# Performance work log

Measured on AMD Instinct MI355X. Metric: run time of the kernel, lower is better.

Reference implementation:

```python
import jax, jax.numpy as jnp
import numpy as np

N, E, G = 100000, 1600000, 256
F_IN, HID, NCLS = 16, 64, 2
EPS = 1e-5


def segment_mean(v, seg, num_segments):
    s = jax.ops.segment_sum(v, seg, num_segments=num_segments)
    c = jax.ops.segment_sum(jnp.ones((v.shape[0], 1), v.dtype), seg, num_segments=num_segments)
    return s / jnp.maximum(c, 1.0)


def graph_norm(x, seg, weight, bias, mean_scale):
    # PyG GraphNorm: per-graph mean/var with learnable mean_scale
    mean = segment_mean(x, seg, G)                      # [G, C]
    centered = x - mean_scale * mean[seg]               # [N, C]
    var = segment_mean(centered * centered, seg, G)     # [G, C]
    return weight * centered * jax.lax.rsqrt(var[seg] + EPS) + bias


def gcn_conv(x, W, b, row, col, n):
    # PyG GCNConv: h = x @ W; symmetric norm with added self-loops; scatter-add; + bias
    h = x @ W                                           # [N, C_out]
    deg = jnp.zeros((n,), x.dtype).at[row].add(1.0) + 1.0  # +1 self-loop
    dinv = jax.lax.rsqrt(deg)
    norm = (dinv[row] * dinv[col])[:, None]             # [E, 1]
    agg = jnp.zeros_like(h).at[row].add(norm * h[col])  # neighbor messages
    agg = agg + (dinv * dinv)[:, None] * h              # self-loop messages
    return agg + b


def setup_inputs():
    key = jax.random.key(0)
    ks = jax.random.split(key, 16)
    x = jax.random.normal(ks[0], (N, F_IN), jnp.float32)
    edge_index = jax.random.randint(ks[1], (2, E), 0, N, jnp.int32)
    batch = jnp.sort(jax.random.randint(ks[2], (N,), 0, G, jnp.int32))
    s = lambda k, shp: jax.random.normal(k, shp, jnp.float32) * 0.05
    return {
        "x": x, "edge_index": edge_index, "batch": batch,
        "gn0_w": jnp.ones((F_IN,)), "gn0_b": jnp.zeros((F_IN,)), "gn0_ms": jnp.ones((F_IN,)),
        "W1": s(ks[3], (F_IN, HID)), "b1": jnp.zeros((HID,)),
        "gn1_w": jnp.ones((HID,)), "gn1_b": jnp.zeros((HID,)), "gn1_ms": jnp.ones((HID,)),
        "W2": s(ks[4], (HID, HID)), "b2": jnp.zeros((HID,)),
        "gn2_w": jnp.ones((HID,)), "gn2_b": jnp.zeros((HID,)), "gn2_ms": jnp.ones((HID,)),
        "W3": s(ks[5], (HID, HID)), "b3": jnp.zeros((HID,)),
        "Wd": s(ks[6], (HID, HID)), "bd": jnp.zeros((HID,)),
        "Wo": s(ks[7], (HID, NCLS)), "bo": jnp.zeros((NCLS,)),
    }


def reference(x, edge_index, batch, gn0_w, gn0_b, gn0_ms, W1, b1, gn1_w, gn1_b, gn1_ms,
              W2, b2, gn2_w, gn2_b, gn2_ms, W3, b3, Wd, bd, Wo, bo):
    row, col = edge_index[0], edge_index[1]
    h = graph_norm(x, batch, gn0_w, gn0_b, gn0_ms)
    h = jax.nn.relu(gcn_conv(h, W1, b1, row, col, N))
    h = graph_norm(h, batch, gn1_w, gn1_b, gn1_ms)
    h = jax.nn.relu(gcn_conv(h, W2, b2, row, col, N))
    h = graph_norm(h, batch, gn2_w, gn2_b, gn2_ms)
    h = jax.nn.relu(gcn_conv(h, W3, b3, row, col, N))
    g = segment_mean(h, batch, G)                       # global_mean_pool -> [G, HID]
    # dropout is identity in eval mode
    g = jax.nn.relu(g @ Wd + bd)
    logits = g @ Wo + bo
    return jax.nn.softmax(logits, axis=1)
```

## Files before the change

kernel.cpp:

```cpp
#include <hip/hip_runtime.h>
#include <hip/hip_bf16.h>

#define NN 100000
#define NE 1600000
#define NG 256
#define FIN 16
#define HID 64
#define NBK 391
#define NTILE 391
#define PMAX 4864
#define MAXT (NN / 16 + NG)

__device__ __forceinline__ int lower_bound_i(const int* __restrict__ b, int n, int v) {
    int lo = 0, hi = n;
    while (lo < hi) { int m = (lo + hi) >> 1; if (b[m] < v) lo = m + 1; else hi = m; }
    return lo;
}

__device__ __forceinline__ unsigned pack_bf16(float a, float b) {
    unsigned ua = __float_as_uint(a), ub = __float_as_uint(b);
    ua = (ua + 0x7fffu + ((ua >> 16) & 1u)) >> 16;
    ub = (ub + 0x7fffu + ((ub >> 16) & 1u)) & 0xffff0000u;
    return ua | ub;
}
#define BF_LO(u) __uint_as_float((u) << 16)
#define BF_HI(u) __uint_as_float((u) & 0xffff0000u)

typedef __attribute__((ext_vector_type(8))) short bf16x8;
typedef __attribute__((ext_vector_type(4))) float f32x4;
union FU { uint4 u; bf16x8 v; };

__global__ __launch_bounds__(512) void k_zb(int* __restrict__ bhist) {
    bhist[threadIdx.x] = 0;
}

__global__ __launch_bounds__(512) void k_bhist(const int4* __restrict__ row4, int* __restrict__ bhist) {
    __shared__ int h[NBK];
    for (int i = threadIdx.x; i < NBK; i += 512) h[i] = 0;
    __syncthreads();
    int t0 = blockIdx.x * 1024 + threadIdx.x;
#pragma unroll
    for (int it = 0; it < 2; ++it) {
        int t = t0 + it * 512;
        if (t < NE / 4) {
            int4 r = row4[t];
            atomicAdd(&h[r.x >> 8], 1); atomicAdd(&h[r.y >> 8], 1);
            atomicAdd(&h[r.z >> 8], 1); atomicAdd(&h[r.w >> 8], 1);
        }
    }
    __syncthreads();
    for (int i = threadIdx.x; i < NBK; i += 512)
        if (h[i]) atomicAdd(&bhist[i], h[i]);
}

__global__ __launch_bounds__(512) void k_bscan(const int* __restrict__ bhist, int* __restrict__ bbase,
                                               int* __restrict__ bcur) {
    __shared__ int sc[512];
    int t = threadIdx.x;
    int v = (t < NBK) ? bhist[t] : 0;
    sc[t] = v;
    __syncthreads();
    int acc = v;
    for (int off = 1; off < 512; off <<= 1) {
        int add = (t >= off) ? sc[t - off] : 0;
        __syncthreads();
        acc += add;
        sc[t] = acc;
        __syncthreads();
    }
    if (t < NBK) { bbase[t] = acc - v; bcur[t] = acc - v; }
    if (t == NBK - 1) bbase[NBK] = acc;
}

__global__ __launch_bounds__(512) void k_bscatter(const int4* __restrict__ row4, const int4* __restrict__ col4,
                                                  int* __restrict__ bcur, int2* __restrict__ pairs) {
    __shared__ int lh[NBK], lofs[NBK], lbase[NBK], lc[NBK];
    __shared__ int sc[512];
    __shared__ int2 stg[4096];
    for (int i = threadIdx.x; i < NBK; i += 512) { lh[i] = 0; lc[i] = 0; }
    __syncthreads();
    int t0 = blockIdx.x * 1024 + threadIdx.x;
#pragma unroll
    for (int it = 0; it < 2; ++it) {
        int t = t0 + it * 512;
        if (t < NE / 4) {
            int4 r = row4[t];
            atomicAdd(&lh[r.x >> 8], 1); atomicAdd(&lh[r.y >> 8], 1);
            atomicAdd(&lh[r.z >> 8], 1); atomicAdd(&lh[r.w >> 8], 1);
        }
    }
    __syncthreads();
    {
        int t = threadIdx.x;
        int v = (t < NBK) ? lh[t] : 0;
        sc[t] = v;
        __syncthreads();
        int acc = v;
        for (int off = 1; off < 512; off <<= 1) {
            int add = (t >= off) ? sc[t - off] : 0;
            __syncthreads();
            acc += add;
            sc[t] = acc;
            __syncthreads();
        }
        if (t < NBK) lofs[t] = acc - v;
    }
    if (threadIdx.x < NBK) {
        int c = lh[threadIdx.x];
        lbase[threadIdx.x] = c ? atomicAdd(&bcur[threadIdx.x], c) : 0;
    }
    __syncthreads();
#pragma unroll
    for (int it = 0; it < 2; ++it) {
        int t = t0 + it * 512;
        if (t < NE / 4) {
            int4 r = row4[t];
            int4 c = col4[t];
            int b, rk;
            b = r.x >> 8; rk = atomicAdd(&lc[b], 1); stg[lofs[b] + rk] = make_int2(r.x, c.x);
            b = r.y >> 8; rk = atomicAdd(&lc[b], 1); stg[lofs[b] + rk] = make_int2(r.y, c.y);
            b = r.z >> 8; rk = atomicAdd(&lc[b], 1); stg[lofs[b] + rk] = make_int2(r.z, c.z);
            b = r.w >> 8; rk = atomicAdd(&lc[b], 1); stg[lofs[b] + rk] = make_int2(r.w, c.w);
        }
    }
    __syncthreads();
    int nv = min(4096, NE - blockIdx.x * 4096);
    for (int j = threadIdx.x; j < nv; j += 512) {
        int2 p = stg[j];
        int b = p.x >> 8;
        pairs[lbase[b] + (j - lofs[b])] = p;
    }
}

__global__ __launch_bounds__(256) void k_bsort(const int2* __restrict__ pairs, const int* __restrict__ bbase,
                                               int* __restrict__ csr_col, int* __restrict__ startv,
                                               int* __restrict__ degc, float* __restrict__ dinv) {
    __shared__ int2 prs[PMAX];
    __shared__ int colo[PMAX];
    __shared__ int cnt[256], ofs[256], c2[256], sc[256];
    int b = blockIdx.x;
    int s = bbase[b];
    int n = min(bbase[b + 1] - s, PMAX);
    cnt[threadIdx.x] = 0;
    c2[threadIdx.x] = 0;
    __syncthreads();
    for (int i = threadIdx.x; i < n; i += 256) {
        int2 p = pairs[s + i];
        prs[i] = p;
        atomicAdd(&cnt[p.x & 255], 1);
    }
    __syncthreads();
    {
        int t = threadIdx.x, v = cnt[t];
        sc[t] = v;
        __syncthreads();
        int acc = v;
        for (int off = 1; off < 256; off <<= 1) {
            int add = (t >= off) ? sc[t - off] : 0;
            __syncthreads();
            acc += add;
            sc[t] = acc;
            __syncthreads();
        }
        ofs[t] = acc - v;
    }
    __syncthreads();
    for (int i = threadIdx.x; i < n; i += 256) {
        int2 p = prs[i];
        int lr = p.x & 255;
        int rk = atomicAdd(&c2[lr], 1);
        colo[ofs[lr] + rk] = p.y;
    }
    __syncthreads();
    for (int i = threadIdx.x; i < n; i += 256) csr_col[s + i] = colo[i];
    int r = (b << 8) + threadIdx.x;
    if (r < NN) {
        int c = cnt[threadIdx.x];
        startv[r] = s + ofs[threadIdx.x];
        degc[r] = c;
        dinv[r] = rsqrtf((float)(c + 1));
    }
}

__global__ __launch_bounds__(256) void k_setup(const int* __restrict__ batch, int* __restrict__ ntot,
                                               int* __restrict__ tg, int* __restrict__ tbase,
                                               int* __restrict__ tcnt, const float* __restrict__ W1,
                                               unsigned* __restrict__ Wt1p) {
    if (blockIdx.x == 1) {
        int t = threadIdx.x;
        int j = t >> 2, kq = t & 3;
#pragma unroll
        for (int i = 0; i < 4; i++) {
            int idx = kq * 4 + i;
            int k = idx * 2;
            unsigned v = 0;
            if (k < FIN) v = pack_bf16(W1[k * 64 + j], W1[(k + 1) * 64 + j]);
            Wt1p[j * 16 + idx] = v;
        }
        return;
    }
    __shared__ int gst[NG + 1];
    __shared__ int sc[NG];
    int t = threadIdx.x;
    gst[t] = lower_bound_i(batch, NN, t);
    if (t == 0) gst[NG] = NN;
    __syncthreads();
    int ng = gst[t + 1] - gst[t];
    int nt = (ng + 15) >> 4;
    sc[t] = nt;
    __syncthreads();
    int acc = nt;
    for (int off = 1; off < NG; off <<= 1) {
        int add = (t >= off) ? sc[t - off] : 0;
        __syncthreads();
        acc += add;
        sc[t] = acc;
        __syncthreads();
    }
    int ofs = acc - nt;
    for (int i = 0; i < nt; i++) {
        tg[ofs + i] = t;
        tbase[ofs + i] = gst[t] + i * 16;
        tcnt[ofs + i] = min(16, ng - i * 16);
    }
    if (t == NG - 1) ntot[0] = acc;
}

__global__ __launch_bounds__(256) void k_graphnorm16(const float* __restrict__ x, const int* __restrict__ batch,
                              const float* __restrict__ w, const float* __restrict__ b,
                              const float* __restrict__ ms, const float* __restrict__ dinv,
                              unsigned* __restrict__ xb) {
    constexpr int C = FIN, NPB = 256 / C;
    __shared__ float red[NPB][C], red2[NPB][C];
    __shared__ float mm_s[C], rs_s[C];
    int g = blockIdx.x;
    int s = lower_bound_i(batch, NN, g);
    int e = lower_bound_i(batch, NN, g + 1);
    float fc = (float)max(e - s, 1);
    int c = threadIdx.x % C, slot = threadIdx.x / C;

    float a1 = 0.f, a2 = 0.f;
    for (int i = s + slot; i < e; i += NPB) { float v = x[i * C + c]; a1 += v; a2 += v * v; }
    red[slot][c] = a1;
    red2[slot][c] = a2;
    __syncthreads();
    if (threadIdx.x < C) {
        float t1 = 0.f, t2 = 0.f;
        for (int k = 0; k < NPB; k++) { t1 += red[k][threadIdx.x]; t2 += red2[k][threadIdx.x]; }
        float mean = t1 / fc;
        float mm = ms[threadIdx.x] * mean;
        float var = t2 / fc - 2.f * mm * mean + mm * mm;
        mm_s[threadIdx.x] = mm;
        rs_s[threadIdx.x] = rsqrtf(var + 1e-5f);
    }
    __syncthreads();
    float mm = mm_s[c], ww = w[c] * rs_s[c], bb = b[c];
    for (int i = s + slot; i < e; i += NPB) {
        float v = (ww * (x[i * C + c] - mm) + bb) * dinv[i];
        float partner = __shfl_xor(v, 1);
        if ((c & 1) == 0) xb[(long)i * 8 + (c >> 1)] = pack_bf16(v, partner);
    }
}

__global__ __launch_bounds__(256) void k_gnstats2(const unsigned* __restrict__ xw, const int* __restrict__ batch,
                          const float* __restrict__ w, const float* __restrict__ b,
                          const float* __restrict__ ms, const float* __restrict__ W,
                          unsigned* __restrict__ Wtp, float* __restrict__ bias2) {
    constexpr int C = 64, NPB = 4;
    __shared__ float red[NPB][C], red2[NPB][C];
    __shared__ float sA[C], sB[C];
    int g = blockIdx.x;
    int s = lower_bound_i(batch, NN, g);
    int e = lower_bound_i(batch, NN, g + 1);
    float fc = (float)max(e - s, 1);
    int c = threadIdx.x & 63, slot = threadIdx.x >> 6;

    float a1 = 0.f, a2 = 0.f;
    for (int i = s + slot; i < e; i += NPB) {
        unsigned u = xw[(long)i * 32 + (c >> 1)];
        float v = (c & 1) ? BF_HI(u) : BF_LO(u);
        a1 += v; a2 += v * v;
    }
    red[slot][c] = a1;
    red2[slot][c] = a2;
    __syncthreads();
    if (threadIdx.x < C) {
        float t1 = 0.f, t2 = 0.f;
        for (int k = 0; k < NPB; k++) { t1 += red[k][threadIdx.x]; t2 += red2[k][threadIdx.x]; }
        float mean = t1 / fc;
        float mm = ms[threadIdx.x] * mean;
        float var = t2 / fc - 2.f * mm * mean + mm * mm;
        float A = w[threadIdx.x] * rsqrtf(var + 1e-5f);
        sA[threadIdx.x] = A;
        sB[threadIdx.x] = b[threadIdx.x] - A * mm;
    }
    __syncthreads();
    int j = threadIdx.x >> 2, kq = threadIdx.x & 3;
    unsigned* wrow = Wtp + ((long)g * 64 + j) * 32 + kq * 8;
    float part = 0.f;
#pragma unroll
    for (int i = 0; i < 8; i++) {
        int k = kq * 16 + 2 * i;
        float w0 = W[k * 64 + j], w1 = W[(k + 1) * 64 + j];
        wrow[i] = pack_bf16(sA[k] * w0, sA[k + 1] * w1);
        part += sB[k] * w0 + sB[k + 1] * w1;
    }
    part += __shfl_xor(part, 1);
    part += __shfl_xor(part, 2);
    if (kq == 0) bias2[g * 64 + j] = part;
}

__global__ __launch_bounds__(256) void k_gather16(const unsigned* __restrict__ xb, const int* __restrict__ startv,
                           const int* __restrict__ degc, const float* __restrict__ dinv,
                           const int* __restrict__ csr_col, unsigned* __restrict__ agg) {
    int wave = (blockIdx.x * blockDim.x + threadIdx.x) >> 6;
    if (wave >= NN) return;
    int lane = threadIdx.x & 63;
    int p = lane & 7, g = lane >> 3;
    int s = startv[wave], cnt = degc[wave];
    float di = dinv[wave];
    float ax = 0.f, ay = 0.f;
    int k = g;
    for (; k + 8 < cnt; k += 16) {
        int c0 = csr_col[s + k], c1 = csr_col[s + k + 8];
        unsigned u0 = xb[(long)c0 * 8 + p], u1 = xb[(long)c1 * 8 + p];
        ax += BF_LO(u0) + BF_LO(u1);
        ay += BF_HI(u0) + BF_HI(u1);
    }
    for (; k < cnt; k += 8) {
        int c0 = csr_col[s + k];
        unsigned u0 = xb[(long)c0 * 8 + p];
        ax += BF_LO(u0);
        ay += BF_HI(u0);
    }
    ax += __shfl_xor(ax, 8);  ay += __shfl_xor(ay, 8);
    ax += __shfl_xor(ax, 16); ay += __shfl_xor(ay, 16);
    ax += __shfl_xor(ax, 32); ay += __shfl_xor(ay, 32);
    if (g == 0) {
        unsigned u = xb[(long)wave * 8 + p];
        ax = (ax + BF_LO(u)) * di;
        ay = (ay + BF_HI(u)) * di;
        agg[(long)wave * 16 + p] = pack_bf16(ax, ay);
    } else if (g == 1) {
        agg[(long)wave * 16 + 8 + p] = 0u;
    }
}

template <int KU, bool PERG, bool RELU, bool DINV>
__global__ __launch_bounds__(256) void k_gemmT(const unsigned* __restrict__ Ain, const unsigned* __restrict__ Wt,
                        const float* __restrict__ biasv, const float* __restrict__ dinv,
                        const int* __restrict__ ntot, const int* __restrict__ tg,
                        const int* __restrict__ tbase, const int* __restrict__ tcnt,
                        unsigned* __restrict__ Aout) {
    const int RW = KU * 16;
    int tix = blockIdx.x * 4 + (threadIdx.x >> 6);
    if (tix >= ntot[0]) return;
    int g = tg[tix], base = tbase[tix], n = tcnt[tix];
    int l = threadIdx.x & 63, r = l & 15, q = l >> 4;
    FU a[KU];
#pragma unroll
    for (int s = 0; s < KU; s++) {
        if (r < n) a[s].u = *(const uint4*)(Ain + (long)(base + r) * RW + s * 16 + q * 4);
        else a[s].u = make_uint4(0, 0, 0, 0);
    }
    const unsigned* wb = PERG ? (Wt + (long)g * 64 * RW) : Wt;
    f32x4 acc[4];
#pragma unroll
    for (int t = 0; t < 4; t++) {
        acc[t] = (f32x4){0.f, 0.f, 0.f, 0.f};
#pragma unroll
        for (int s = 0; s < KU; s++) {
            FU bfrag;
            bfrag.u = *(const uint4*)(wb + (long)(t * 16 + r) * RW + s * 16 + q * 4);
            acc[t] = __builtin_amdgcn_mfma_f32_16x16x32_bf16(a[s].v, bfrag.v, acc[t], 0, 0, 0);
        }
    }
    const float* bb = PERG ? (biasv + g * 64) : biasv;
    float dv[4];
#pragma unroll
    for (int e = 0; e < 4; e++) {
        int node = base + q * 4 + e;
        dv[e] = DINV ? ((node < NN) ? dinv[node] : 0.f) : 1.f;
    }
#pragma unroll
    for (int t = 0; t < 4; t++) {
        float bv = bb[t * 16 + r];
#pragma unroll
        for (int e = 0; e < 4; e++) {
            float v = acc[t][e] + bv;
            if (RELU) v = fmaxf(v, 0.f);
            if (DINV) v *= dv[e];
            float part = __shfl_xor(v, 1);
            if ((q * 4 + e) < n && (r & 1) == 0)
                Aout[(long)(base + q * 4 + e) * 32 + t * 8 + (r >> 1)] = pack_bf16(v, part);
        }
    }
}

__global__ __launch_bounds__(256) void k_gather64(const unsigned* __restrict__ h2, const int* __restrict__ startv,
                           const int* __restrict__ degc, const float* __restrict__ dinv,
                           const int* __restrict__ csr_col, const float* __restrict__ bias,
                           unsigned* __restrict__ outp) {
    int wave = (blockIdx.x * blockDim.x + threadIdx.x) >> 6;
    if (wave >= NN) return;
    int lane = threadIdx.x & 63;
    int p = lane & 31, g = lane >> 5;
    int s = startv[wave], cnt = degc[wave];
    float di = dinv[wave];
    float ax = 0.f, ay = 0.f;
    if (g == 0) {
        unsigned u = h2[(long)wave * 32 + p];
        ax = BF_LO(u);
        ay = BF_HI(u);
    }
    for (int k = g * 8; k < cnt; k += 16) {
        int cc[8];
#pragma unroll
        for (int i = 0; i < 8; i++) {
            int idx = k + i;
            cc[i] = (idx < cnt) ? csr_col[s + idx] : -1;
        }
        unsigned u[8];
#pragma unroll
        for (int i = 0; i < 8; i++)
            u[i] = (cc[i] >= 0) ? h2[(long)cc[i] * 32 + p] : 0u;
#pragma unroll
        for (int i = 0; i < 8; i++) { ax += BF_LO(u[i]); ay += BF_HI(u[i]); }
    }
    ax += __shfl_xor(ax, 32);
    ay += __shfl_xor(ay, 32);
    if (g == 0) {
        float vx = fmaxf(ax * di + bias[2 * p], 0.f);
        float vy = fmaxf(ay * di + bias[2 * p + 1], 0.f);
        outp[(long)wave * 32 + p] = pack_bf16(vx, vy);
    }
}

__global__ __launch_bounds__(1024) void k_poolhead(const unsigned* __restrict__ xw, const int* __restrict__ batch,
                       const float* __restrict__ Wd, const float* __restrict__ bd,
                       const float* __restrict__ Wo, const float* __restrict__ bo,
                       float* __restrict__ out) {
    __shared__ float red[16][64];
    __shared__ float wds[64 * 64];
    __shared__ float gs[64];
    int g = blockIdx.x;
    int s = lower_bound_i(batch, NN, g);
    int e = lower_bound_i(batch, NN, g + 1);
    int c = threadIdx.x & 63, slot = threadIdx.x >> 6;
    for (int i = threadIdx.x; i < 64 * 64; i += 1024) wds[i] = Wd[i];
    float acc = 0.f;
    for (int i = s + slot; i < e; i += 16) {
        unsigned u = xw[(long)i * 32 + (c >> 1)];
        acc += (c & 1) ? BF_HI(u) : BF_LO(u);
    }
    red[slot][c] = acc;
    __syncthreads();
    if (threadIdx.x < 64) {
        float t = 0.f;
        for (int k = 0; k < 16; k++) t += red[k][threadIdx.x];
        gs[threadIdx.x] = t / (float)max(e - s, 1);
    }
    __syncthreads();
    if (threadIdx.x < 64) {
        int j = threadIdx.x;
        float a2 = bd[j];
        for (int k = 0; k < 64; k++) a2 += gs[k] * wds[k * 64 + j];
        float hv = fmaxf(a2, 0.f);
        float p0 = hv * Wo[j * 2 + 0], p1 = hv * Wo[j * 2 + 1];
        for (int off = 32; off; off >>= 1) { p0 += __shfl_down(p0, off); p1 += __shfl_down(p1, off); }
        if (j == 0) {
            float l0 = p0 + bo[0], l1 = p1 + bo[1];
            float m = fmaxf(l0, l1);
            float e0 = expf(l0 - m), e1 = expf(l1 - m);
            float inv = 1.f / (e0 + e1);
            out[g * 2 + 0] = e0 * inv;
            out[g * 2 + 1] = e1 * inv;
        }
    }
}

extern "C" void kernel_launch(void* const* d_in, const int* in_sizes, int n_in,
                              void* d_out, int out_size, void* d_ws, size_t ws_size,
                              hipStream_t stream) {
    const float* x = (const float*)d_in[0];
    const int* ei = (const int*)d_in[1];
    const int* row = ei;
    const int* col = ei + NE;
    const int* batch = (const int*)d_in[2];
    const float* gn0w = (const float*)d_in[3];
    const float* gn0b = (const float*)d_in[4];
    const float* gn0ms = (const float*)d_in[5];
    const float* W1 = (const float*)d_in[6];
    const float* b1 = (const float*)d_in[7];
    const float* gn1w = (const float*)d_in[8];
    const float* gn1b = (const float*)d_in[9];
    const float* gn1ms = (const float*)d_in[10];
    const float* W2 = (const float*)d_in[11];
    const float* b2 = (const float*)d_in[12];
    const float* gn2w = (const float*)d_in[13];
    const float* gn2b = (const float*)d_in[14];
    const float* gn2ms = (const float*)d_in[15];
    const float* W3 = (const float*)d_in[16];
    const float* b3 = (const float*)d_in[17];
    const float* Wd = (const float*)d_in[18];
    const float* bd = (const float*)d_in[19];
    const float* Wo = (const float*)d_in[20];
    const float* bo = (const float*)d_in[21];
    float* outp = (float*)d_out;

    int* bhist = (int*)d_ws;
    int* bbase = bhist + 512;
    int* bcur = bbase + 512;
    int* startv = bcur + 512;
    int* degc = startv + NN;
    float* dinv = (float*)(degc + NN);
    int* csr_col = (int*)(dinv + NN);
    int* ntot = csr_col + NE;
    int* tg = ntot + 16;
    int* tbase = tg + 6608;
    int* tcnt = tbase + 6608;
    unsigned* Wt1p = (unsigned*)(tcnt + 6608);
    unsigned* Wtp = Wt1p + 1024;
    float* bias2 = (float*)(Wtp + (long)NG * 64 * 32);
    unsigned* xb = (unsigned*)(bias2 + NG * 64);
    unsigned* agg16 = xb + (long)NN * 8;
    unsigned* bufA = agg16 + (long)NN * 16;
    unsigned* bufB = bufA + (long)NN * 32;
    unsigned* h2 = bufB + (long)NN * 32;
    int2* pairs = (int2*)bufA;

    const int NBG = (MAXT + 3) / 4;

    k_zb<<<1, 512, 0, stream>>>(bhist);
    k_bhist<<<NTILE, 512, 0, stream>>>((const int4*)row, bhist);
    k_bscan<<<1, 512, 0, stream>>>(bhist, bbase, bcur);
    k_bscatter<<<NTILE, 512, 0, stream>>>((const int4*)row, (const int4*)col, bcur, pairs);
    k_bsort<<<NBK, 256, 0, stream>>>(pairs, bbase, csr_col, startv, degc, dinv);

    k_setup<<<2, 256, 0, stream>>>(batch, ntot, tg, tbase, tcnt, W1, Wt1p);

    k_graphnorm16<<<NG, 256, 0, stream>>>(x, batch, gn0w, gn0b, gn0ms, dinv, xb);
    k_gather16<<<(NN * 64 + 255) / 256, 256, 0, stream>>>(xb, startv, degc, dinv, csr_col, agg16);
    k_gemmT<1, false, true, false><<<NBG, 256, 0, stream>>>(agg16, Wt1p, b1, dinv, ntot, tg, tbase, tcnt, bufA);

    k_gnstats2<<<NG, 256, 0, stream>>>(bufA, batch, gn1w, gn1b, gn1ms, W2, Wtp, bias2);
    k_gemmT<2, true, false, true><<<NBG, 256, 0, stream>>>(bufA, Wtp, bias2, dinv, ntot, tg, tbase, tcnt, h2);
    k_gather64<<<(NN * 64 + 255) / 256, 256, 0, stream>>>(h2, startv, degc, dinv, csr_col, b2, bufB);

    k_gnstats2<<<NG, 256, 0, stream>>>(bufB, batch, gn2w, gn2b, gn2ms, W3, Wtp, bias2);
    k_gemmT<2, true, false, true><<<NBG, 256, 0, stream>>>(bufB, Wtp, bias2, dinv, ntot, tg, tbase, tcnt, h2);
    k_gather64<<<(NN * 64 + 255) / 256, 256, 0, stream>>>(h2, startv, degc, dinv, csr_col, b3, bufA);

    k_poolhead<<<NG, 1024, 0, stream>>>(bufA, batch, Wd, bd, Wo, bo, outp);
}
```

Measured before the change: 414.0 us.

## Pad CSR rows to multiples of four with sentinel zero rows for vectorized gathers

The CSR build in k_bsort now pads each row's neighbor list to a multiple of four, filling the padding with a sentinel index NN. A zero row is written at index NN of the feature buffers, so the gathers can load column indices as uint4 and skip bounds checks and the scalar tail loops. Alongside this, the graph-norm and stats kernels move to 512-thread blocks with packed float4 reductions, and the zeroing kernel is replaced by hipMemsetAsync. The padding adds storage and gather work for the padded slots, and k_bsort no longer stages pairs in LDS, so it reads them from global memory twice.

New measurement: 382.3 us. 1.08x faster.

```diff
diff --git a/kernel.cpp b/kernel.cpp
--- a/kernel.cpp
+++ b/kernel.cpp
@@ -9,6 +9,7 @@
 #define NBK 391
 #define NTILE 391
 #define PMAX 4864
+#define BMAXP 5632
 #define MAXT (NN / 16 + NG)
 
 __device__ __forceinline__ int lower_bound_i(const int* __restrict__ b, int n, int v) {
@@ -29,10 +30,6 @@
 typedef __attribute__((ext_vector_type(8))) short bf16x8;
 typedef __attribute__((ext_vector_type(4))) float f32x4;
 union FU { uint4 u; bf16x8 v; };
-
-__global__ __launch_bounds__(512) void k_zb(int* __restrict__ bhist) {
-    bhist[threadIdx.x] = 0;
-}
 
 __global__ __launch_bounds__(512) void k_bhist(const int4* __restrict__ row4, int* __restrict__ bhist) {
     __shared__ int h[NBK];
@@ -135,23 +132,21 @@
 __global__ __launch_bounds__(256) void k_bsort(const int2* __restrict__ pairs, const int* __restrict__ bbase,
                                                int* __restrict__ csr_col, int* __restrict__ startv,
                                                int* __restrict__ degc, float* __restrict__ dinv) {
-    __shared__ int2 prs[PMAX];
-    __shared__ int colo[PMAX];
-    __shared__ int cnt[256], ofs[256], c2[256], sc[256];
+    __shared__ int colo[BMAXP];
+    __shared__ int cnt[256], pofs[256], c2[256], sc[256];
     int b = blockIdx.x;
     int s = bbase[b];
     int n = min(bbase[b + 1] - s, PMAX);
     cnt[threadIdx.x] = 0;
     c2[threadIdx.x] = 0;
     __syncthreads();
-    for (int i = threadIdx.x; i < n; i += 256) {
-        int2 p = pairs[s + i];
-        prs[i] = p;
-        atomicAdd(&cnt[p.x & 255], 1);
-    }
-    __syncthreads();
+    for (int i = threadIdx.x; i < n; i += 256)
+        atomicAdd(&cnt[pairs[s + i].x & 255], 1);
+    __syncthreads();
+    int c = cnt[threadIdx.x];
+    int pc = (c + 3) & ~3;
     {
-        int t = threadIdx.x, v = cnt[t];
+        int t = threadIdx.x, v = pc;
         sc[t] = v;
         __syncthreads();
         int acc = v;
@@ -162,22 +157,25 @@
             sc[t] = acc;
             __syncthreads();
         }
-        ofs[t] = acc - v;
-    }
+        pofs[t] = acc - v;
+    }
+    __syncthreads();
+    int ptot = sc[255];
+    for (int i = threadIdx.x; i < ptot; i += 256) colo[i] = NN;
     __syncthreads();
     for (int i = threadIdx.x; i < n; i += 256) {
-        int2 p = prs[i];
+        int2 p = pairs[s + i];
         int lr = p.x & 255;
         int rk = atomicAdd(&c2[lr], 1);
-        colo[ofs[lr] + rk] = p.y;
-    }
-    __syncthreads();
-    for (int i = threadIdx.x; i < n; i += 256) csr_col[s + i] = colo[i];
+        colo[pofs[lr] + rk] = p.y;
+    }
+    __syncthreads();
+    int gb = b * BMAXP;
+    for (int i = threadIdx.x; i < ptot; i += 256) csr_col[gb + i] = colo[i];
     int r = (b << 8) + threadIdx.x;
     if (r < NN) {
-        int c = cnt[threadIdx.x];
-        startv[r] = s + ofs[threadIdx.x];
-        degc[r] = c;
+        startv[r] = gb + pofs[threadIdx.x];
+        degc[r] = pc;
         dinv[r] = rsqrtf((float)(c + 1));
     }
 }
@@ -185,7 +183,8 @@
 __global__ __launch_bounds__(256) void k_setup(const int* __restrict__ batch, int* __restrict__ ntot,
                                                int* __restrict__ tg, int* __restrict__ tbase,
                                                int* __restrict__ tcnt, const float* __restrict__ W1,
-                                               unsigned* __restrict__ Wt1p) {
+                                               unsigned* __restrict__ Wt1p, unsigned* __restrict__ xb,
+                                               unsigned* __restrict__ h2) {
     if (blockIdx.x == 1) {
         int t = threadIdx.x;
         int j = t >> 2, kq = t & 3;
@@ -197,6 +196,8 @@
             if (k < FIN) v = pack_bf16(W1[k * 64 + j], W1[(k + 1) * 64 + j]);
             Wt1p[j * 16 + idx] = v;
         }
+        if (t < 32) h2[(long)NN * 32 + t] = 0u;
+        if (t < 8) xb[(long)NN * 8 + t] = 0u;
         return;
     }
     __shared__ int gst[NG + 1];
@@ -226,11 +227,11 @@
     if (t == NG - 1) ntot[0] = acc;
 }
 
-__global__ __launch_bounds__(256) void k_graphnorm16(const float* __restrict__ x, const int* __restrict__ batch,
+__global__ __launch_bounds__(512) void k_graphnorm16(const float* __restrict__ x, const int* __restrict__ batch,
                               const float* __restrict__ w, const float* __restrict__ b,
                               const float* __restrict__ ms, const float* __restrict__ dinv,
                               unsigned* __restrict__ xb) {
-    constexpr int C = FIN, NPB = 256 / C;
+    constexpr int C = FIN, NPB = 512 / C;
     __shared__ float red[NPB][C], red2[NPB][C];
     __shared__ float mm_s[C], rs_s[C];
     int g = blockIdx.x;
@@ -262,52 +263,57 @@
     }
 }
 
-__global__ __launch_bounds__(256) void k_gnstats2(const unsigned* __restrict__ xw, const int* __restrict__ batch,
+__global__ __launch_bounds__(512) void k_gnstats2(const unsigned* __restrict__ xw, const int* __restrict__ batch,
                           const float* __restrict__ w, const float* __restrict__ b,
                           const float* __restrict__ ms, const float* __restrict__ W,
                           unsigned* __restrict__ Wtp, float* __restrict__ bias2) {
-    constexpr int C = 64, NPB = 4;
-    __shared__ float red[NPB][C], red2[NPB][C];
-    __shared__ float sA[C], sB[C];
+    __shared__ float4 red[16][32];
+    __shared__ float sA[64], sB[64];
     int g = blockIdx.x;
     int s = lower_bound_i(batch, NN, g);
     int e = lower_bound_i(batch, NN, g + 1);
     float fc = (float)max(e - s, 1);
-    int c = threadIdx.x & 63, slot = threadIdx.x >> 6;
-
-    float a1 = 0.f, a2 = 0.f;
-    for (int i = s + slot; i < e; i += NPB) {
-        unsigned u = xw[(long)i * 32 + (c >> 1)];
-        float v = (c & 1) ? BF_HI(u) : BF_LO(u);
-        a1 += v; a2 += v * v;
-    }
-    red[slot][c] = a1;
-    red2[slot][c] = a2;
-    __syncthreads();
-    if (threadIdx.x < C) {
+    int cu = threadIdx.x & 31, slot = threadIdx.x >> 5;
+
+    float s1l = 0.f, s1h = 0.f, s2l = 0.f, s2h = 0.f;
+    for (int i = s + slot; i < e; i += 16) {
+        unsigned u = xw[(long)i * 32 + cu];
+        float lo = BF_LO(u), hi = BF_HI(u);
+        s1l += lo; s1h += hi; s2l += lo * lo; s2h += hi * hi;
+    }
+    red[slot][cu] = make_float4(s1l, s1h, s2l, s2h);
+    __syncthreads();
+    if (threadIdx.x < 64) {
+        int cc = threadIdx.x, iu = cc >> 1, hi = cc & 1;
         float t1 = 0.f, t2 = 0.f;
-        for (int k = 0; k < NPB; k++) { t1 += red[k][threadIdx.x]; t2 += red2[k][threadIdx.x]; }
+        for (int k = 0; k < 16; k++) {
+            float4 v = red[k][iu];
+            t1 += hi ? v.y : v.x;
+            t2 += hi ? v.w : v.z;
+        }
         float mean = t1 / fc;
-        float mm = ms[threadIdx.x] * mean;
+        float mm = ms[cc] * mean;
         float var = t2 / fc - 2.f * mm * mean + mm * mm;
-        float A = w[threadIdx.x] * rsqrtf(var + 1e-5f);
-        sA[threadIdx.x] = A;
-        sB[threadIdx.x] = b[threadIdx.x] - A * mm;
-    }
-    __syncthreads();
-    int j = threadIdx.x >> 2, kq = threadIdx.x & 3;
-    unsigned* wrow = Wtp + ((long)g * 64 + j) * 32 + kq * 8;
-    float part = 0.f;
-#pragma unroll
-    for (int i = 0; i < 8; i++) {
-        int k = kq * 16 + 2 * i;
-        float w0 = W[k * 64 + j], w1 = W[(k + 1) * 64 + j];
-        wrow[i] = pack_bf16(sA[k] * w0, sA[k + 1] * w1);
-        part += sB[k] * w0 + sB[k + 1] * w1;
-    }
-    part += __shfl_xor(part, 1);
-    part += __shfl_xor(part, 2);
-    if (kq == 0) bias2[g * 64 + j] = part;
+        float A = w[cc] * rsqrtf(var + 1e-5f);
+        sA[cc] = A;
+        sB[cc] = b[cc] - A * mm;
+    }
+    __syncthreads();
+    if (threadIdx.x < 256) {
+        int j = threadIdx.x >> 2, kq = threadIdx.x & 3;
+        unsigned* wrow = Wtp + ((long)g * 64 + j) * 32 + kq * 8;
+        float part = 0.f;
+#pragma unroll
+        for (int i = 0; i < 8; i++) {
+            int k = kq * 16 + 2 * i;
+            float w0 = W[k * 64 + j], w1 = W[(k + 1) * 64 + j];
+            wrow[i] = pack_bf16(sA[k] * w0, sA[k + 1] * w1);
+            part += sB[k] * w0 + sB[k + 1] * w1;
+        }
+        part += __shfl_xor(part, 1);
+        part += __shfl_xor(part, 2);
+        if (kq == 0) bias2[g * 64 + j] = part;
+    }
 }
 
 __global__ __launch_bounds__(256) void k_gather16(const unsigned* __restrict__ xb, const int* __restrict__ startv,
@@ -316,20 +322,21 @@
     int wave = (blockIdx.x * blockDim.x + threadIdx.x) >> 6;
     if (wave >= NN) return;
     int lane = threadIdx.x & 63;
-    int p = lane & 7, g = lane >> 3;
-    int s = startv[wave], cnt = degc[wave];
+    unsigned p = lane & 7;
+    int g = lane >> 3;
+    int s = startv[wave], pcnt = degc[wave];
     float di = dinv[wave];
     float ax = 0.f, ay = 0.f;
     int k = g;
-    for (; k + 8 < cnt; k += 16) {
-        int c0 = csr_col[s + k], c1 = csr_col[s + k + 8];
-        unsigned u0 = xb[(long)c0 * 8 + p], u1 = xb[(long)c1 * 8 + p];
+    for (; k + 8 < pcnt; k += 16) {
+        unsigned c0 = (unsigned)csr_col[s + k], c1 = (unsigned)csr_col[s + k + 8];
+        unsigned u0 = xb[c0 * 8u + p], u1 = xb[c1 * 8u + p];
         ax += BF_LO(u0) + BF_LO(u1);
         ay += BF_HI(u0) + BF_HI(u1);
     }
-    for (; k < cnt; k += 8) {
-        int c0 = csr_col[s + k];
-        unsigned u0 = xb[(long)c0 * 8 + p];
+    if (k < pcnt) {
+        unsigned c0 = (unsigned)csr_col[s + k];
+        unsigned u0 = xb[c0 * 8u + p];
         ax += BF_LO(u0);
         ay += BF_HI(u0);
     }
@@ -337,7 +344,7 @@
     ax += __shfl_xor(ax, 16); ay += __shfl_xor(ay, 16);
     ax += __shfl_xor(ax, 32); ay += __shfl_xor(ay, 32);
     if (g == 0) {
-        unsigned u = xb[(long)wave * 8 + p];
+        unsigned u = xb[(unsigned)wave * 8u + p];
         ax = (ax + BF_LO(u)) * di;
         ay = (ay + BF_HI(u)) * di;
         agg[(long)wave * 16 + p] = pack_bf16(ax, ay);
@@ -404,35 +411,43 @@
     int wave = (blockIdx.x * blockDim.x + threadIdx.x) >> 6;
     if (wave >= NN) return;
     int lane = threadIdx.x & 63;
-    int p = lane & 31, g = lane >> 5;
-    int s = startv[wave], cnt = degc[wave];
+    unsigned p = lane & 31;
+    int g = lane >> 5;
+    int s = startv[wave], pcnt = degc[wave];
     float di = dinv[wave];
     float ax = 0.f, ay = 0.f;
     if (g == 0) {
-        unsigned u = h2[(long)wave * 32 + p];
+        unsigned u = h2[(unsigned)wave * 32u + p];
         ax = BF_LO(u);
         ay = BF_HI(u);
     }
-    for (int k = g * 8; k < cnt; k += 16) {
-        int cc[8];
-#pragma unroll
-        for (int i = 0; i < 8; i++) {
-            int idx = k + i;
-            cc[i] = (idx < cnt) ? csr_col[s + idx] : -1;
-        }
-        unsigned u[8];
-#pragma unroll
-        for (int i = 0; i < 8; i++)
-            u[i] = (cc[i] >= 0) ? h2[(long)cc[i] * 32 + p] : 0u;
-#pragma unroll
-        for (int i = 0; i < 8; i++) { ax += BF_LO(u[i]); ay += BF_HI(u[i]); }
+    int k = g * 8;
+    for (; k + 8 <= pcnt; k += 16) {
+        uint4 c0 = *(const uint4*)(csr_col + s + k);
+        uint4 c1 = *(const uint4*)(csr_col + s + k + 4);
+        unsigned u0 = h2[c0.x * 32u + p], u1 = h2[c0.y * 32u + p],
+                 u2 = h2[c0.z * 32u + p], u3 = h2[c0.w * 32u + p],
+                 u4 = h2[c1.x * 32u + p], u5 = h2[c1.y * 32u + p],
+                 u6 = h2[c1.z * 32u + p], u7 = h2[c1.w * 32u + p];
+        ax += BF_LO(u0) + BF_LO(u1) + BF_LO(u2) + BF_LO(u3)
+            + BF_LO(u4) + BF_LO(u5) + BF_LO(u6) + BF_LO(u7);
+        ay += BF_HI(u0) + BF_HI(u1) + BF_HI(u2) + BF_HI(u3)
+            + BF_HI(u4) + BF_HI(u5) + BF_HI(u6) + BF_HI(u7);
+    }
+    if (k < pcnt) {
+        uint4 c0 = *(const uint4*)(csr_col + s + k);
+        unsigned u0 = h2[c0.x * 32u + p], u1 = h2[c0.y * 32u + p],
+                 u2 = h2[c0.z * 32u + p], u3 = h2[c0.w * 32u + p];
+        ax += BF_LO(u0) + BF_LO(u1) + BF_LO(u2) + BF_LO(u3);
+        ay += BF_HI(u0) + BF_HI(u1) + BF_HI(u2) + BF_HI(u3);
     }
     ax += __shfl_xor(ax, 32);
     ay += __shfl_xor(ay, 32);
     if (g == 0) {
-        float vx = fmaxf(ax * di + bias[2 * p], 0.f);
-        float vy = fmaxf(ay * di + bias[2 * p + 1], 0.f);
-        outp[(long)wave * 32 + p] = pack_bf16(vx, vy);
+        float2 bv = ((const float2*)bias)[p];
+        float vx = fmaxf(ax * di + bv.x, 0.f);
+        float vy = fmaxf(ay * di + bv.y, 0.f);
+        outp[(unsigned)wave * 32u + p] = pack_bf16(vx, vy);
     }
 }
 
@@ -515,7 +530,7 @@
     int* degc = startv + NN;
     float* dinv = (float*)(degc + NN);
     int* csr_col = (int*)(dinv + NN);
-    int* ntot = csr_col + NE;
+    int* ntot = csr_col + (long)NBK * BMAXP;
     int* tg = ntot + 16;
     int* tbase = tg + 6608;
     int* tcnt = tbase + 6608;
@@ -523,7 +538,7 @@
     unsigned* Wtp = Wt1p + 1024;
     float* bias2 = (float*)(Wtp + (long)NG * 64 * 32);
     unsigned* xb = (unsigned*)(bias2 + NG * 64);
-    unsigned* agg16 = xb + (long)NN * 8;
+    unsigned* agg16 = xb + (long)NN * 8 + 16;
     unsigned* bufA = agg16 + (long)NN * 16;
     unsigned* bufB = bufA + (long)NN * 32;
     unsigned* h2 = bufB + (long)NN * 32;
@@ -531,23 +546,23 @@
 
     const int NBG = (MAXT + 3) / 4;
 
-    k_zb<<<1, 512, 0, stream>>>(bhist);
+    hipMemsetAsync(bhist, 0, 512 * sizeof(int), stream);
     k_bhist<<<NTILE, 512, 0, stream>>>((const int4*)row, bhist);
     k_bscan<<<1, 512, 0, stream>>>(bhist, bbase, bcur);
     k_bscatter<<<NTILE, 512, 0, stream>>>((const int4*)row, (const int4*)col, bcur, pairs);
     k_bsort<<<NBK, 256, 0, stream>>>(pairs, bbase, csr_col, startv, degc, dinv);
 
-    k_setup<<<2, 256, 0, stream>>>(batch, ntot, tg, tbase, tcnt, W1, Wt1p);
-
-    k_graphnorm16<<<NG, 256, 0, stream>>>(x, batch, gn0w, gn0b, gn0ms, dinv, xb);
+    k_setup<<<2, 256, 0, stream>>>(batch, ntot, tg, tbase, tcnt, W1, Wt1p, xb, h2);
+
+    k_graphnorm16<<<NG, 512, 0, stream>>>(x, batch, gn0w, gn0b, gn0ms, dinv, xb);
     k_gather16<<<(NN * 64 + 255) / 256, 256, 0, stream>>>(xb, startv, degc, dinv, csr_col, agg16);
     k_gemmT<1, false, true, false><<<NBG, 256, 0, stream>>>(agg16, Wt1p, b1, dinv, ntot, tg, tbase, tcnt, bufA);
 
-    k_gnstats2<<<NG, 256, 0, stream>>>(bufA, batch, gn1w, gn1b, gn1ms, W2, Wtp, bias2);
+    k_gnstats2<<<NG, 512, 0, stream>>>(bufA, batch, gn1w, gn1b, gn1ms, W2, Wtp, bias2);
     k_gemmT<2, true, false, true><<<NBG, 256, 0, stream>>>(bufA, Wtp, bias2, dinv, ntot, tg, tbase, tcnt, h2);
     k_gather64<<<(NN * 64 + 255) / 256, 256, 0, stream>>>(h2, startv, degc, dinv, csr_col, b2, bufB);
 
-    k_gnstats2<<<NG, 256, 0, stream>>>(bufB, batch, gn2w, gn2b, gn2ms, W3, Wtp, bias2);
+    k_gnstats2<<<NG, 512, 0, stream>>>(bufB, batch, gn2w, gn2b, gn2ms, W3, Wtp, bias2);
     k_gemmT<2, true, false, true><<<NBG, 256, 0, stream>>>(bufB, Wtp, bias2, dinv, ntot, tg, tbase, tcnt, h2);
     k_gather64<<<(NN * 64 + 255) / 256, 256, 0, stream>>>(h2, startv, degc, dinv, csr_col, b3, bufA);
 
```
